# Optimization experiments

Measured on AMD Instinct MI355X. Metric: run time of the kernel, lower is better.

Reference implementation:

```python
import jax, jax.numpy as jnp
import numpy as np

BS, N, DEG = 2, 16384, 16
NE = N * DEG          # 262144 edges
D = 128               # node/edge feature dim
S = 4                 # number of completed blocks
EPS = 1e-6


def mlp(x, W1, b1, W2, b2):
    # MLP(in, hidden=128, out, act=SiLU, layer_norm=False)
    return jax.nn.silu(x @ W1 + b1) @ W2 + b2


def rms_norm(x, w):
    return x * jax.lax.rsqrt(jnp.mean(x * x, axis=-1, keepdims=True) + EPS) * w


def setup_inputs() -> dict:
    key = jax.random.key(0)
    ks = jax.random.split(key, 14)
    f32 = jnp.float32
    sc = 0.05
    return {
        "V": jax.random.normal(ks[0], (BS, N, D), f32),
        "E": jax.random.normal(ks[1], (BS, NE, D), f32),
        "blocks": jax.random.normal(ks[2], (S, BS, N, D), f32),
        "We1": jax.random.normal(ks[3], (3 * D, D), f32) * sc,
        "be1": jnp.zeros((D,), f32),
        "We2": jax.random.normal(ks[4], (D, D), f32) * sc,
        "be2": jnp.zeros((D,), f32),
        "Wn1": jax.random.normal(ks[5], (2 * D, D), f32) * sc,
        "bn1": jnp.zeros((D,), f32),
        "Wn2": jax.random.normal(ks[6], (D, D), f32) * sc,
        "bn2": jnp.zeros((D,), f32),
        "w_attn": jax.random.normal(ks[7], (D,), f32) * sc,
        "rms_w": jnp.ones((D,), f32),
        "edges": jax.random.randint(ks[8], (BS, NE, 2), 0, N, jnp.int32),
    }


def reference(V, E, blocks, We1, be1, We2, be2, Wn1, bn1, Wn2, bn2,
              w_attn, rms_w, edges):
    # ---- GNN layer: edge gather -> edge MLP -> scatter_mean -> node MLP ----
    senders = jnp.take_along_axis(V, edges[..., 0][:, :, None], axis=1)    # [b,E,D]
    receivers = jnp.take_along_axis(V, edges[..., 1][:, :, None], axis=1)  # [b,E,D]
    edge_inpt = jnp.concatenate([senders, receivers, E], axis=-1)          # [b,E,3D]
    edge_emb = mlp(edge_inpt, We1, be1, We2, be2)                          # [b,E,D]
    e0, e1 = jnp.split(edge_emb, 2, axis=-1)                               # [b,E,D/2] each

    def seg_mean(vals, idx):
        s = jax.ops.segment_sum(vals, idx, num_segments=N)
        c = jax.ops.segment_sum(jnp.ones(idx.shape, vals.dtype), idx,
                                num_segments=N)
        return s / jnp.maximum(c, 1.0)[:, None]

    m0 = jax.vmap(seg_mean)(e0, edges[..., 0])   # [b,N,D/2]
    m1 = jax.vmap(seg_mean)(e1, edges[..., 1])   # [b,N,D/2]
    node_inpt = jnp.concatenate([V, m0, m1], axis=-1)                      # [b,N,2D]
    node_emb = mlp(node_inpt, Wn1, bn1, Wn2, bn2)                          # [b,N,D]

    # ---- block_attn_res: depth-wise attention over stacked blocks ----
    Vs = jnp.concatenate([blocks, node_emb[None]], axis=0)                 # [S+1,b,N,D]
    K = rms_norm(Vs, rms_w)
    logits = jnp.einsum('d,sbnd->sbn', w_attn, K)
    alpha = jax.nn.softmax(logits, axis=0)
    h = jnp.einsum('sbn,sbnd->bnd', alpha, Vs)                             # [b,N,D]
    return h
```

## Files before the change

kernel.cpp:

```cpp
#include <hip/hip_runtime.h>
#include <hip/hip_bf16.h>

#define D 128
#define NNODES 16384
#define NEDGES 262144
#define NBATCH 2
#define TE 64

typedef __attribute__((ext_vector_type(8))) short bf16x8;
typedef __attribute__((ext_vector_type(4))) float f32x4;

__device__ __forceinline__ unsigned short f2bf(float f) {
    unsigned int u = __float_as_uint(f);
    unsigned int r = (u + 0x7fffu + ((u >> 16) & 1u)) >> 16;
    return (unsigned short)r;
}

__device__ __forceinline__ unsigned int pk2bf(float lo, float hi) {
    return (unsigned int)f2bf(lo) | ((unsigned int)f2bf(hi) << 16);
}

__device__ __forceinline__ float bf2f(unsigned short u) {
    return __uint_as_float(((unsigned int)u) << 16);
}

__device__ __forceinline__ bf16x8 pack8(f32x4 a, f32x4 b) {
    unsigned int w0 = pk2bf(a[0], a[1]);
    unsigned int w1 = pk2bf(a[2], a[3]);
    unsigned int w2 = pk2bf(b[0], b[1]);
    unsigned int w3 = pk2bf(b[2], b[3]);
    typedef __attribute__((ext_vector_type(4))) unsigned int u32x4;
    u32x4 u; u.x = w0; u.y = w1; u.z = w2; u.w = w3;
    return __builtin_bit_cast(bf16x8, u);
}

__global__ __launch_bounds__(256)
void prep_weights(const float* __restrict__ We1, const float* __restrict__ We2,
                  const float* __restrict__ Wn1, const float* __restrict__ Wn2,
                  unsigned short* __restrict__ w)
{
    int id = blockIdx.x * 256 + threadIdx.x;
    if (id < 16384) {
        int e = id & 7, l = (id >> 3) & 63, nblk = (id >> 9) & 7, ks = id >> 12;
        int k = 256 + ks * 32 + ((l >> 4) & 3) * 8 + e;
        int col = nblk * 16 + (l & 15);
        w[id] = f2bf(We1[k * 128 + col]);
    } else if (id < 32768) {
        int i2 = id - 16384;
        int e = i2 & 7, l = (i2 >> 3) & 63, nblk = (i2 >> 9) & 7, ks = i2 >> 12;
        int k = ks * 32 + ((l >> 4) & 3) * 8 + e;
        int col = nblk * 16 + (l & 15);
        w[id] = f2bf(We2[k * 128 + col]);
    } else if (id < 65536) {
        int i3 = id - 32768;
        int j = i3 >> 7, k = i3 & 127;
        int row = (j < 128) ? k : (128 + k);
        w[id] = f2bf(We1[row * 128 + (j & 127)]);
    } else if (id < 98304) {
        int i4 = id - 65536;
        int n = i4 >> 8, k = i4 & 255;
        w[id] = f2bf(Wn1[k * 128 + n]);
    } else {
        int i5 = id - 98304;
        int n = i5 >> 7, k = i5 & 127;
        w[id] = f2bf(Wn2[k * 128 + n]);
    }
}

__global__ __launch_bounds__(256)
void partial_kernel(const float* __restrict__ V, const unsigned short* __restrict__ wp,
                    unsigned short* __restrict__ P)
{
    __shared__ unsigned short smem[64 * 136];
    const int t = threadIdx.x, lane = t & 63, wave = t >> 6;
    const int l15 = lane & 15, l4 = lane >> 4;
    const long long r0 = (long long)blockIdx.x * 64;

    for (int i = t; i < 64 * 32; i += 256) {
        int c4 = i & 31, r = i >> 5;
        float4 v = *(const float4*)(V + (r0 + r) * 128 + c4 * 4);
        uint2 p; p.x = pk2bf(v.x, v.y); p.y = pk2bf(v.z, v.w);
        *(uint2*)(&smem[r * 136 + c4 * 4]) = p;
    }
    __syncthreads();

    const int j0 = wave * 64;
    f32x4 acc[4][4] = {};
    const unsigned short* bb0 = wp + (j0 + l15) * 128 + l4 * 8;
    #pragma unroll
    for (int ks = 0; ks < 4; ++ks) {
        bf16x8 bb[4];
        #pragma unroll
        for (int n = 0; n < 4; ++n)
            bb[n] = *(const bf16x8*)(bb0 + n * 16 * 128 + ks * 32);
        #pragma unroll
        for (int mq = 0; mq < 4; ++mq) {
            bf16x8 a = *(const bf16x8*)(&smem[(mq * 16 + l15) * 136 + l4 * 8 + ks * 32]);
            #pragma unroll
            for (int n = 0; n < 4; ++n)
                acc[mq][n] = __builtin_amdgcn_mfma_f32_16x16x32_bf16(a, bb[n], acc[mq][n], 0, 0, 0);
        }
    }
    #pragma unroll
    for (int mq = 0; mq < 4; ++mq) {
        #pragma unroll
        for (int n = 0; n < 4; ++n) {
            #pragma unroll
            for (int i = 0; i < 4; ++i) {
                int row = mq * 16 + l4 * 4 + i;
                int col = j0 + n * 16 + l15;
                P[(r0 + row) * 256 + col] = f2bf(acc[mq][n][i]);
            }
        }
    }
}

__global__ __launch_bounds__(256)
void edge_kernel(const float* __restrict__ E, const int* __restrict__ edges,
                 const unsigned short* __restrict__ P,
                 const unsigned short* __restrict__ w1ef, const float* __restrict__ be1,
                 const unsigned short* __restrict__ w2f, const float* __restrict__ be2,
                 float* __restrict__ m0sum, float* __restrict__ m1sum,
                 float* __restrict__ c0, float* __restrict__ c1)
{
    __shared__ unsigned short Hbuf[TE * 136];

    const int t    = threadIdx.x;
    const int lane = t & 63;
    const int wave = t >> 6;
    const int wr   = wave >> 1;
    const int wc   = wave & 1;
    const int l15  = lane & 15;
    const int l4   = lane >> 4;

    const long long eflat0 = (long long)blockIdx.x * TE;
    const int b  = (int)(eflat0 / NEDGES);
    const long long nb0 = (long long)b * NNODES;

    if (t < TE) {
        int2 e2 = *(const int2*)(edges + (eflat0 + t) * 2);
        atomicAdd(&c0[nb0 + e2.x], 1.f);
        atomicAdd(&c1[nb0 + e2.y], 1.f);
    }

    f32x4 acc[2][4] = {};
    {
        const float* er0 = E + (eflat0 + wr * 32 + l15) * D + l4 * 8;
        #pragma unroll
        for (int ks = 0; ks < 4; ++ks) {
            f32x4 xa0 = *(const f32x4*)(er0 + ks * 32);
            f32x4 xb0 = *(const f32x4*)(er0 + ks * 32 + 4);
            f32x4 xa1 = *(const f32x4*)(er0 + 16 * D + ks * 32);
            f32x4 xb1 = *(const f32x4*)(er0 + 16 * D + ks * 32 + 4);
            bf16x8 a0 = pack8(xa0, xb0);
            bf16x8 a1 = pack8(xa1, xb1);
            #pragma unroll
            for (int n = 0; n < 4; ++n) {
                bf16x8 bb = *(const bf16x8*)(w1ef + (((ks * 8 + wc * 4 + n) * 64 + lane) << 3));
                acc[0][n] = __builtin_amdgcn_mfma_f32_16x16x32_bf16(a0, bb, acc[0][n], 0, 0, 0);
                acc[1][n] = __builtin_amdgcn_mfma_f32_16x16x32_bf16(a1, bb, acc[1][n], 0, 0, 0);
            }
        }
    }

    int nd0[2][4], nd1[2][4];
    #pragma unroll
    for (int m = 0; m < 2; ++m) {
        #pragma unroll
        for (int i = 0; i < 4; ++i) {
            int row = wr * 32 + m * 16 + l4 * 4 + i;
            int2 e2 = *(const int2*)(edges + (eflat0 + row) * 2);
            nd0[m][i] = e2.x;
            nd1[m][i] = e2.y;
        }
    }

    #pragma unroll
    for (int n = 0; n < 4; ++n) {
        int col = wc * 64 + n * 16 + l15;
        float bias = be1[col];
        #pragma unroll
        for (int m = 0; m < 2; ++m) {
            #pragma unroll
            for (int i = 0; i < 4; ++i) {
                int row = wr * 32 + m * 16 + l4 * 4 + i;
                float a = acc[m][n][i] + bias
                        + bf2f(P[(nb0 + nd0[m][i]) * 256 + col])
                        + bf2f(P[(nb0 + nd1[m][i]) * 256 + 128 + col]);
                Hbuf[row * 136 + col] = f2bf(a / (1.f + __expf(-a)));
            }
        }
    }
    __syncthreads();

    f32x4 acc2[2][4] = {};
    {
        const unsigned short* hrow = &Hbuf[(wr * 32 + l15) * 136 + l4 * 8];
        #pragma unroll
        for (int ks = 0; ks < 4; ++ks) {
            bf16x8 a0 = *(const bf16x8*)(hrow + ks * 32);
            bf16x8 a1 = *(const bf16x8*)(hrow + 16 * 136 + ks * 32);
            #pragma unroll
            for (int n = 0; n < 4; ++n) {
                bf16x8 bb = *(const bf16x8*)(w2f + (((ks * 8 + wc * 4 + n) * 64 + lane) << 3));
                acc2[0][n] = __builtin_amdgcn_mfma_f32_16x16x32_bf16(a0, bb, acc2[0][n], 0, 0, 0);
                acc2[1][n] = __builtin_amdgcn_mfma_f32_16x16x32_bf16(a1, bb, acc2[1][n], 0, 0, 0);
            }
        }
    }

    {
        float* dst_arr = wc ? m1sum : m0sum;
        #pragma unroll
        for (int n = 0; n < 4; ++n) {
            int colh = n * 16 + l15;
            float bias = be2[wc * 64 + colh];
            #pragma unroll
            for (int m = 0; m < 2; ++m) {
                #pragma unroll
                for (int i = 0; i < 4; ++i) {
                    int node = wc ? nd1[m][i] : nd0[m][i];
                    atomicAdd(dst_arr + (nb0 + node) * 64 + colh,
                              acc2[m][n][i] + bias);
                }
            }
        }
    }
}

__global__ __launch_bounds__(256)
void node_kernel(const float* __restrict__ V,
                 const float* __restrict__ m0sum, const float* __restrict__ m1sum,
                 const float* __restrict__ c0, const float* __restrict__ c1,
                 const unsigned short* __restrict__ wn1t, const float* __restrict__ bn1,
                 const unsigned short* __restrict__ wn2t, const float* __restrict__ bn2,
                 float* __restrict__ node_emb)
{
    __shared__ unsigned short smem[TE * 264];

    const int t    = threadIdx.x;
    const int lane = t & 63;
    const int wave = t >> 6;
    const int wr   = wave >> 1;
    const int wc   = wave & 1;
    const int l15  = lane & 15;
    const int l4   = lane >> 4;

    const long long nflat0 = (long long)blockIdx.x * TE;

    for (int i = t; i < TE * 64; i += 256) {
        int c4 = i & 63;
        int n  = i >> 6;
        long long node = nflat0 + n;
        float4 v; int off;
        if (c4 < 32) {
            v = *(const float4*)(V + node * 128 + c4 * 4);
            off = c4 * 4;
        } else if (c4 < 48) {
            v = *(const float4*)(m0sum + node * 64 + (c4 - 32) * 4);
            float inv = 1.f / fmaxf(c0[node], 1.f);
            v.x *= inv; v.y *= inv; v.z *= inv; v.w *= inv;
            off = 128 + (c4 - 32) * 4;
        } else {
            v = *(const float4*)(m1sum + node * 64 + (c4 - 48) * 4);
            float inv = 1.f / fmaxf(c1[node], 1.f);
            v.x *= inv; v.y *= inv; v.z *= inv; v.w *= inv;
            off = 192 + (c4 - 48) * 4;
        }
        uint2 p;
        p.x = pk2bf(v.x, v.y);
        p.y = pk2bf(v.z, v.w);
        *(uint2*)(&smem[n * 264 + c4 * 4]) = p;
    }
    __syncthreads();

    f32x4 acc[2][4] = {};
    {
        const unsigned short* arow = &smem[(wr * 32 + l15) * 264 + l4 * 8];
        const unsigned short* bb0  = wn1t + (wc * 64 + l15) * 256 + l4 * 8;
        for (int ks = 0; ks < 8; ++ks) {
            bf16x8 a0 = *(const bf16x8*)(arow + ks * 32);
            bf16x8 a1 = *(const bf16x8*)(arow + 16 * 264 + ks * 32);
            #pragma unroll
            for (int n = 0; n < 4; ++n) {
                bf16x8 bb = *(const bf16x8*)(bb0 + n * 16 * 256 + ks * 32);
                acc[0][n] = __builtin_amdgcn_mfma_f32_16x16x32_bf16(a0, bb, acc[0][n], 0, 0, 0);
                acc[1][n] = __builtin_amdgcn_mfma_f32_16x16x32_bf16(a1, bb, acc[1][n], 0, 0, 0);
            }
        }
    }
    __syncthreads();

    #pragma unroll
    for (int n = 0; n < 4; ++n) {
        int col = wc * 64 + n * 16 + l15;
        float bias = bn1[col];
        #pragma unroll
        for (int m = 0; m < 2; ++m) {
            #pragma unroll
            for (int i = 0; i < 4; ++i) {
                int row = wr * 32 + m * 16 + l4 * 4 + i;
                float a = acc[m][n][i] + bias;
                smem[row * 136 + col] = f2bf(a / (1.f + __expf(-a)));
            }
        }
    }
    __syncthreads();

    f32x4 acc2[2][4] = {};
    {
        const unsigned short* hrow = &smem[(wr * 32 + l15) * 136 + l4 * 8];
        const unsigned short* bb0  = wn2t + (wc * 64 + l15) * 128 + l4 * 8;
        #pragma unroll
        for (int ks = 0; ks < 4; ++ks) {
            bf16x8 a0 = *(const bf16x8*)(hrow + ks * 32);
            bf16x8 a1 = *(const bf16x8*)(hrow + 16 * 136 + ks * 32);
            #pragma unroll
            for (int n = 0; n < 4; ++n) {
                bf16x8 bb = *(const bf16x8*)(bb0 + n * 16 * 128 + ks * 32);
                acc2[0][n] = __builtin_amdgcn_mfma_f32_16x16x32_bf16(a0, bb, acc2[0][n], 0, 0, 0);
                acc2[1][n] = __builtin_amdgcn_mfma_f32_16x16x32_bf16(a1, bb, acc2[1][n], 0, 0, 0);
            }
        }
    }

    #pragma unroll
    for (int n = 0; n < 4; ++n) {
        int col = wc * 64 + n * 16 + l15;
        float bias = bn2[col];
        #pragma unroll
        for (int m = 0; m < 2; ++m) {
            #pragma unroll
            for (int i = 0; i < 4; ++i) {
                long long row = nflat0 + wr * 32 + m * 16 + l4 * 4 + i;
                node_emb[row * 128 + col] = acc2[m][n][i] + bias;
            }
        }
    }
}

__global__ __launch_bounds__(256)
void attn_kernel(const float* __restrict__ blocks, const float* __restrict__ node_emb,
                 const float* __restrict__ w_attn, const float* __restrict__ rms_w,
                 float* __restrict__ out)
{
    const int t    = threadIdx.x;
    const int wave = t >> 6;
    const int lane = t & 63;
    const long long node = (long long)blockIdx.x * 4 + wave;
    const int d0 = lane * 2;

    float2 wa = *(const float2*)(w_attn + d0);
    float2 rw = *(const float2*)(rms_w + d0);

    float xs[5][2];
    float lg[5];
    #pragma unroll
    for (int s = 0; s < 5; ++s) {
        const float* src = (s < 4)
            ? (blocks + ((long long)s * NBATCH * NNODES + node) * 128)
            : (node_emb + node * 128);
        float2 x = *(const float2*)(src + d0);
        xs[s][0] = x.x; xs[s][1] = x.y;
        float ss = x.x * x.x + x.y * x.y;
        float wv = wa.x * rw.x * x.x + wa.y * rw.y * x.y;
        #pragma unroll
        for (int m = 1; m < 64; m <<= 1) {
            ss += __shfl_xor(ss, m);
            wv += __shfl_xor(wv, m);
        }
        lg[s] = wv * rsqrtf(ss * (1.f / 128.f) + 1e-6f);
    }

    float mx = lg[0];
    #pragma unroll
    for (int s = 1; s < 5; ++s) mx = fmaxf(mx, lg[s]);
    float ex[5], sum = 0.f;
    #pragma unroll
    for (int s = 0; s < 5; ++s) { ex[s] = __expf(lg[s] - mx); sum += ex[s]; }
    float inv = 1.f / sum;

    float h0 = 0.f, h1 = 0.f;
    #pragma unroll
    for (int s = 0; s < 5; ++s) {
        float a = ex[s] * inv;
        h0 = fmaf(a, xs[s][0], h0);
        h1 = fmaf(a, xs[s][1], h1);
    }
    *(float2*)(out + node * 128 + d0) = make_float2(h0, h1);
}

extern "C" void kernel_launch(void* const* d_in, const int* in_sizes, int n_in,
                              void* d_out, int out_size, void* d_ws, size_t ws_size,
                              hipStream_t stream)
{
    const float* V      = (const float*)d_in[0];
    const float* E      = (const float*)d_in[1];
    const float* blocks = (const float*)d_in[2];
    const float* We1    = (const float*)d_in[3];
    const float* be1    = (const float*)d_in[4];
    const float* We2    = (const float*)d_in[5];
    const float* be2    = (const float*)d_in[6];
    const float* Wn1    = (const float*)d_in[7];
    const float* bn1    = (const float*)d_in[8];
    const float* Wn2    = (const float*)d_in[9];
    const float* bn2    = (const float*)d_in[10];
    const float* w_attn = (const float*)d_in[11];
    const float* rms_w  = (const float*)d_in[12];
    const int*   edges  = (const int*)d_in[13];
    float* out = (float*)d_out;

    float* ws = (float*)d_ws;
    float* m0sum    = ws;
    float* m1sum    = m0sum + 2097152;
    float* c0       = m1sum + 2097152;
    float* c1       = c0 + 32768;
    float* node_emb = c1 + 32768;
    unsigned short* wbf = (unsigned short*)(node_emb + 4194304);
    unsigned short* w1ef = wbf;
    unsigned short* w2f  = wbf + 16384;
    unsigned short* wp   = wbf + 32768;
    unsigned short* wn1t = wbf + 65536;
    unsigned short* wn2t = wbf + 98304;
    unsigned short* P    = wbf + 114688;

    (void)hipMemsetAsync(d_ws, 0, (size_t)(2097152 * 2 + 32768 * 2) * sizeof(float), stream);

    prep_weights<<<448, 256, 0, stream>>>(We1, We2, Wn1, Wn2, wbf);

    partial_kernel<<<(NBATCH * NNODES) / 64, 256, 0, stream>>>(V, wp, P);

    edge_kernel<<<(NBATCH * NEDGES) / TE, 256, 0, stream>>>(
        E, edges, P, w1ef, be1, w2f, be2, m0sum, m1sum, c0, c1);

    node_kernel<<<(NBATCH * NNODES) / TE, 256, 0, stream>>>(
        V, m0sum, m1sum, c0, c1, wn1t, bn1, wn2t, bn2, node_emb);

    attn_kernel<<<(NBATCH * NNODES) / 4, 256, 0, stream>>>(
        blocks, node_emb, w_attn, rms_w, out);
}
```

Before: 378.5 us.

## Scatter edge messages with packed bf16 atomics and apply bias after mean

The edge kernel's scatter now accumulates into bf16 buffers using the packed global_atomic_pk_add_bf16 instruction. Adjacent lanes are combined with a shuffle so each atomic carries two columns, which halves the atomic count and the accumulator memory. The be2 bias is removed from the per-edge atomics and added once per node in the node kernel, only when the count is at least one. The trade-off is bf16 accumulation precision, since sums of around 16 values each lose accuracy, and the node kernel's load loop is restructured.

```diff
diff --git a/kernel.cpp b/kernel.cpp
--- a/kernel.cpp
+++ b/kernel.cpp
@@ -32,6 +32,10 @@
     typedef __attribute__((ext_vector_type(4))) unsigned int u32x4;
     u32x4 u; u.x = w0; u.y = w1; u.z = w2; u.w = w3;
     return __builtin_bit_cast(bf16x8, u);
+}
+
+__device__ __forceinline__ void atomic_pk(unsigned int* p, unsigned int v) {
+    asm volatile("global_atomic_pk_add_bf16 %0, %1, off" :: "v"(p), "v"(v) : "memory");
 }
 
 __global__ __launch_bounds__(256)
@@ -119,8 +123,8 @@
 void edge_kernel(const float* __restrict__ E, const int* __restrict__ edges,
                  const unsigned short* __restrict__ P,
                  const unsigned short* __restrict__ w1ef, const float* __restrict__ be1,
-                 const unsigned short* __restrict__ w2f, const float* __restrict__ be2,
-                 float* __restrict__ m0sum, float* __restrict__ m1sum,
+                 const unsigned short* __restrict__ w2f,
+                 unsigned short* __restrict__ us_m0, unsigned short* __restrict__ us_m1,
                  float* __restrict__ c0, float* __restrict__ c1)
 {
     __shared__ unsigned short Hbuf[TE * 136];
@@ -210,18 +214,21 @@
     }
 
     {
-        float* dst_arr = wc ? m1sum : m0sum;
+        unsigned short* dst_arr = wc ? us_m1 : us_m0;
         #pragma unroll
         for (int n = 0; n < 4; ++n) {
             int colh = n * 16 + l15;
-            float bias = be2[wc * 64 + colh];
             #pragma unroll
             for (int m = 0; m < 2; ++m) {
                 #pragma unroll
                 for (int i = 0; i < 4; ++i) {
                     int node = wc ? nd1[m][i] : nd0[m][i];
-                    atomicAdd(dst_arr + (nb0 + node) * 64 + colh,
-                              acc2[m][n][i] + bias);
+                    float v  = acc2[m][n][i];
+                    float vn = __shfl_xor(v, 1);
+                    if (!(lane & 1)) {
+                        atomic_pk((unsigned int*)(dst_arr + (nb0 + node) * 64 + colh),
+                                  pk2bf(v, vn));
+                    }
                 }
             }
         }
@@ -230,8 +237,9 @@
 
 __global__ __launch_bounds__(256)
 void node_kernel(const float* __restrict__ V,
-                 const float* __restrict__ m0sum, const float* __restrict__ m1sum,
+                 const unsigned short* __restrict__ m0, const unsigned short* __restrict__ m1,
                  const float* __restrict__ c0, const float* __restrict__ c1,
+                 const float* __restrict__ be2,
                  const unsigned short* __restrict__ wn1t, const float* __restrict__ bn1,
                  const unsigned short* __restrict__ wn2t, const float* __restrict__ bn2,
                  float* __restrict__ node_emb)
@@ -248,29 +256,34 @@
 
     const long long nflat0 = (long long)blockIdx.x * TE;
 
-    for (int i = t; i < TE * 64; i += 256) {
-        int c4 = i & 63;
-        int n  = i >> 6;
+    for (int i = t; i < TE * 48; i += 256) {
+        int n  = i / 48;
+        int c4 = i - n * 48;
         long long node = nflat0 + n;
-        float4 v; int off;
         if (c4 < 32) {
-            v = *(const float4*)(V + node * 128 + c4 * 4);
-            off = c4 * 4;
-        } else if (c4 < 48) {
-            v = *(const float4*)(m0sum + node * 64 + (c4 - 32) * 4);
-            float inv = 1.f / fmaxf(c0[node], 1.f);
-            v.x *= inv; v.y *= inv; v.z *= inv; v.w *= inv;
-            off = 128 + (c4 - 32) * 4;
+            float4 v = *(const float4*)(V + node * 128 + c4 * 4);
+            uint2 p; p.x = pk2bf(v.x, v.y); p.y = pk2bf(v.z, v.w);
+            *(uint2*)(&smem[n * 264 + c4 * 4]) = p;
         } else {
-            v = *(const float4*)(m1sum + node * 64 + (c4 - 48) * 4);
-            float inv = 1.f / fmaxf(c1[node], 1.f);
-            v.x *= inv; v.y *= inv; v.z *= inv; v.w *= inv;
-            off = 192 + (c4 - 48) * 4;
-        }
-        uint2 p;
-        p.x = pk2bf(v.x, v.y);
-        p.y = pk2bf(v.z, v.w);
-        *(uint2*)(&smem[n * 264 + c4 * 4]) = p;
+            int dir = (c4 >= 40);
+            int j = c4 - 32 - dir * 8;
+            const unsigned short* src = dir ? m1 : m0;
+            float cnt = (dir ? c1 : c0)[node];
+            float inv = 1.f / fmaxf(cnt, 1.f);
+            float bon = (cnt >= 1.f) ? 1.f : 0.f;
+            uint4 raw = *(const uint4*)(src + node * 64 + j * 8);
+            const float* bb = be2 + dir * 64 + j * 8;
+            unsigned int rr[4] = {raw.x, raw.y, raw.z, raw.w};
+            unsigned int o[4];
+            #pragma unroll
+            for (int q = 0; q < 4; ++q) {
+                float lo = bf2f((unsigned short)(rr[q] & 0xffffu)) * inv + bb[2 * q] * bon;
+                float hi = bf2f((unsigned short)(rr[q] >> 16)) * inv + bb[2 * q + 1] * bon;
+                o[q] = pk2bf(lo, hi);
+            }
+            uint4 st; st.x = o[0]; st.y = o[1]; st.z = o[2]; st.w = o[3];
+            *(uint4*)(&smem[n * 264 + 128 + dir * 64 + j * 8]) = st;
+        }
     }
     __syncthreads();
 
@@ -410,10 +423,9 @@
     const int*   edges  = (const int*)d_in[13];
     float* out = (float*)d_out;
 
-    float* ws = (float*)d_ws;
-    float* m0sum    = ws;
-    float* m1sum    = m0sum + 2097152;
-    float* c0       = m1sum + 2097152;
+    unsigned short* us_m0 = (unsigned short*)d_ws;
+    unsigned short* us_m1 = us_m0 + 2097152;
+    float* c0       = (float*)(us_m1 + 2097152);
     float* c1       = c0 + 32768;
     float* node_emb = c1 + 32768;
     unsigned short* wbf = (unsigned short*)(node_emb + 4194304);
@@ -424,17 +436,17 @@
     unsigned short* wn2t = wbf + 98304;
     unsigned short* P    = wbf + 114688;
 
-    (void)hipMemsetAsync(d_ws, 0, (size_t)(2097152 * 2 + 32768 * 2) * sizeof(float), stream);
+    (void)hipMemsetAsync(d_ws, 0, (size_t)(2097152 * 2 * 2 + 32768 * 2 * 4), stream);
 
     prep_weights<<<448, 256, 0, stream>>>(We1, We2, Wn1, Wn2, wbf);
 
     partial_kernel<<<(NBATCH * NNODES) / 64, 256, 0, stream>>>(V, wp, P);
 
     edge_kernel<<<(NBATCH * NEDGES) / TE, 256, 0, stream>>>(
-        E, edges, P, w1ef, be1, w2f, be2, m0sum, m1sum, c0, c1);
+        E, edges, P, w1ef, be1, w2f, us_m0, us_m1, c0, c1);
 
     node_kernel<<<(NBATCH * NNODES) / TE, 256, 0, stream>>>(
-        V, m0sum, m1sum, c0, c1, wn1t, bn1, wn2t, bn2, node_emb);
+        V, us_m0, us_m1, c0, c1, be2, wn1t, bn1, wn2t, bn2, node_emb);
 
     attn_kernel<<<(NBATCH * NNODES) / 4, 256, 0, stream>>>(
         blocks, node_emb, w_attn, rms_w, out);
```

Measured after the change: 376.5 us. Within noise of the previous version (-0.5%).
